# Kernel optimization log

Measured on AMD Instinct MI355X. Metric: run time of the kernel, lower is better.

Reference implementation:

```python
import jax, jax.numpy as jnp
import numpy as np

N_ENT = 50000
N_REL = 500
N_DIM = 256
K = 4            # num_blocks; n_arity = 3 -> arch has K**3 = 64 entries
B = 1024


def setup_inputs() -> dict:
    key = jax.random.key(0)
    k0, k1, k2, k3 = jax.random.split(key, 4)
    facts = jax.random.randint(k0, (B, 3), 0, N_REL)          # head, tail, rela (all < n_rel <= n_ent)
    arch = jax.random.randint(k1, (K ** 3,), 0, 3)            # selects op in {0, 1, -1}
    ent_w = jax.random.normal(k2, (N_ENT, N_DIM), dtype=jnp.float32) * 0.05  # xavier-ish scale
    rel_w = jax.random.normal(k3, (N_REL, N_DIM), dtype=jnp.float32) * 0.05
    return {
        "facts": facts,
        "arch": arch,
        "ent_w": ent_w,
        "rel_w": rel_w,
        "bne_gamma": jnp.ones((N_DIM,), jnp.float32),
        "bne_beta": jnp.zeros((N_DIM,), jnp.float32),
        "bnr_gamma": jnp.ones((N_DIM,), jnp.float32),
        "bnr_beta": jnp.zeros((N_DIM,), jnp.float32),
    }


def _bn(x, gamma, beta, eps=1e-5):
    # BatchNorm1d in training mode: biased batch statistics over the batch dim.
    m = jnp.mean(x, axis=0)
    v = jnp.var(x, axis=0)
    return (x - m) * jax.lax.rsqrt(v + eps) * gamma + beta


def _bce(p, y):
    # torch F.binary_cross_entropy clamps log terms at -100
    logp = jnp.maximum(jnp.log(p), -100.0)
    log1mp = jnp.maximum(jnp.log1p(-p), -100.0)
    return -jnp.mean(y * logp + (1.0 - y) * log1mp)


def reference(facts, arch, ent_w, rel_w, bne_gamma, bne_beta, bnr_gamma, bnr_beta):
    L = N_DIM // K
    h, t, r = facts[:, 0], facts[:, 1], facts[:, 2]
    # separate BN calls for head / tail batches, as in the torch code (dropout is eval-mode identity)
    he = _bn(ent_w[h], bne_gamma, bne_beta).reshape(-1, K, L)   # [B, K, L]
    te = _bn(ent_w[t], bne_gamma, bne_beta).reshape(-1, K, L)
    re = _bn(rel_w[r], bnr_gamma, bnr_beta).reshape(-1, K, L)
    # alpha[i,j,k] = ops[op_idx[i*K*K + j*K + k]] in {0, 1, -1}
    alpha = jnp.asarray([0.0, 1.0, -1.0], dtype=ent_w.dtype)[arch].reshape(K, K, K)
    # fused extend + inner_vec + inner_alpha_bi + sum-over-blocks:
    # last_idx=2 (head side, rela x tail): vec[b,k,l] = sum_{i,j} alpha[i,j,k] r[b,i,l] t[b,j,l]
    head_vec = jnp.einsum('ijk,bil,bjl->bkl', alpha, re, te).reshape(-1, N_DIM)
    # last_idx=1 (tail side, rela x head): vec[b,k,l] = sum_{i,j} alpha[i,k,j] r[b,i,l] h[b,j,l]
    tail_vec = jnp.einsum('ikj,bil,bjl->bkl', alpha, re, he).reshape(-1, N_DIM)
    head_p = jax.nn.softmax(head_vec @ ent_w.T, axis=1)         # [B, N_ENT]
    tail_p = jax.nn.softmax(tail_vec @ ent_w.T, axis=1)
    head_label = jax.nn.one_hot(h, N_ENT, dtype=head_p.dtype)
    tail_label = jax.nn.one_hot(t, N_ENT, dtype=tail_p.dtype)
    return _bce(head_p, head_label) + _bce(tail_p, tail_label)
```

## Files before the change

### kernel.cpp

```cpp
#include <hip/hip_runtime.h>

#define N_ENT   50000
#define N_ENT_P 50048
#define NDIM    256
#define BATCH   1024
#define MROWS   2048
#define BM      128
#define BN      128
#define BK      64
#define NTILES  391
#define NSTRIP  32
#define SHIFT   30.0f

typedef __attribute__((ext_vector_type(8))) short short8;
typedef __attribute__((ext_vector_type(4))) float f32x4;

__device__ __forceinline__ unsigned short f2bf(float f) {
  unsigned int u = __float_as_uint(f);
  u += 0x7fffu + ((u >> 16) & 1u);
  return (unsigned short)(u >> 16);
}

__device__ __forceinline__ void async16(const void* g, void* lds) {
  __builtin_amdgcn_global_load_lds(
      (const __attribute__((address_space(1))) unsigned int*)g,
      (__attribute__((address_space(3))) unsigned int*)lds,
      16, 0, 0);
}

__global__ void k_convert(const float* __restrict__ ent_w,
                          unsigned short* __restrict__ Wb) {
  int t = blockIdx.x * 256 + threadIdx.x;
  int row = t >> 6, c4 = (t & 63) << 2;
  ushort4 v;
  if (row < N_ENT) {
    float4 f = *(const float4*)(ent_w + row * NDIM + c4);
    v.x = f2bf(f.x); v.y = f2bf(f.y); v.z = f2bf(f.z); v.w = f2bf(f.w);
  } else {
    v.x = v.y = v.z = v.w = 0;
  }
  *(ushort4*)(Wb + row * NDIM + c4) = v;
}

__global__ void k_stats(const int* __restrict__ facts,
                        const float* __restrict__ ent_w,
                        const float* __restrict__ rel_w,
                        float* __restrict__ stats) {
  int seg = blockIdx.y;
  int d = threadIdx.x;
  const float* tab = (seg == 2) ? rel_w : ent_w;
  int r0 = blockIdx.x * 16;
  int idxs[16];
#pragma unroll
  for (int i = 0; i < 16; ++i) idxs[i] = facts[(r0 + i) * 3 + seg];
  float s = 0.f, s2 = 0.f;
#pragma unroll
  for (int i = 0; i < 16; ++i) {
    float v = tab[idxs[i] * NDIM + d];
    s += v; s2 += v * v;
  }
  atomicAdd(&stats[(seg * 2 + 0) * NDIM + d], s);
  atomicAdd(&stats[(seg * 2 + 1) * NDIM + d], s2);
}

__global__ void k_vectors(const int* __restrict__ facts, const int* __restrict__ arch,
                          const float* __restrict__ ent_w, const float* __restrict__ rel_w,
                          const float* __restrict__ bne_g, const float* __restrict__ bne_b,
                          const float* __restrict__ bnr_g, const float* __restrict__ bnr_b,
                          const float* __restrict__ stats,
                          unsigned short* __restrict__ HVb, float* __restrict__ zlab) {
  __shared__ float sh_he[256], sh_te[256], sh_re[256], sh_alpha[64], sh_red[16];
  int b = blockIdx.x, d = threadIdx.x;
  int h = facts[b * 3 + 0], t = facts[b * 3 + 1], r = facts[b * 3 + 2];
  const float inv = 1.0f / (float)BATCH;
  float mh = stats[0 * 256 + d] * inv, vh = stats[1 * 256 + d] * inv - mh * mh;
  float mt = stats[2 * 256 + d] * inv, vt = stats[3 * 256 + d] * inv - mt * mt;
  float mr = stats[4 * 256 + d] * inv, vr = stats[5 * 256 + d] * inv - mr * mr;
  float sch = rsqrtf(vh + 1e-5f) * bne_g[d], shh = bne_b[d] - mh * sch;
  float sct = rsqrtf(vt + 1e-5f) * bne_g[d], sht = bne_b[d] - mt * sct;
  float scr = rsqrtf(vr + 1e-5f) * bnr_g[d], shr = bnr_b[d] - mr * scr;
  sh_he[d] = ent_w[h * NDIM + d] * sch + shh;
  sh_te[d] = ent_w[t * NDIM + d] * sct + sht;
  sh_re[d] = rel_w[r * NDIM + d] * scr + shr;
  if (d < 64) {
    int a = arch[d];
    sh_alpha[d] = (a == 0) ? 0.f : ((a == 1) ? 1.f : -1.f);
  }
  __syncthreads();
  int k = d >> 6, l = d & 63;
  float hv = 0.f, tv = 0.f;
#pragma unroll
  for (int i = 0; i < 4; ++i) {
    float re_i = sh_re[i * 64 + l];
#pragma unroll
    for (int j = 0; j < 4; ++j) {
      hv += sh_alpha[i * 16 + j * 4 + k] * re_i * sh_te[j * 64 + l];
      tv += sh_alpha[i * 16 + k * 4 + j] * re_i * sh_he[j * 64 + l];
    }
  }
  HVb[b * NDIM + d] = f2bf(hv);
  HVb[(BATCH + b) * NDIM + d] = f2bf(tv);
  float ph = hv * ent_w[h * NDIM + d];
  float pt = tv * ent_w[t * NDIM + d];
  for (int m = 1; m < 64; m <<= 1) { ph += __shfl_xor(ph, m); pt += __shfl_xor(pt, m); }
  int wid = d >> 6;
  if ((d & 63) == 0) { sh_red[wid] = ph; sh_red[8 + wid] = pt; }
  __syncthreads();
  if (d == 0) {
    zlab[b] = sh_red[0] + sh_red[1] + sh_red[2] + sh_red[3];
    zlab[BATCH + b] = sh_red[8] + sh_red[9] + sh_red[10] + sh_red[11];
  }
}

__global__ void __launch_bounds__(256, 2)
k_gemm(const unsigned short* __restrict__ HVb, const unsigned short* __restrict__ Wb,
       float* __restrict__ m1, float* __restrict__ m2) {
  __shared__ __align__(16) unsigned short As[BM * BK];
  __shared__ __align__(16) unsigned short Bs[BN * BK];
  const int tid = threadIdx.x;
  const int lane = tid & 63, wid = tid >> 6;
  const int L = blockIdx.x;
  const int xcd = L & 7, r = L >> 3;
  const int strip = xcd * 4 + (r >> 4);
  const int bm = (r & 15) * BM;
  const int wm = (wid & 1) * 64, wn = (wid >> 1) * 64;
  const int q = lane >> 4, ln = lane & 15;

  float ps1[4][4] = {}, ps2[4][4] = {};

  for (int nt = strip; nt < NTILES; nt += NSTRIP) {
    const int bn = nt * BN;
    f32x4 acc[4][4] = {};
    for (int kc = 0; kc < NDIM; kc += BK) {
      __syncthreads();
#pragma unroll
      for (int c = 0; c < 4; ++c) {
        int G = (wid * 4 + c) * 64 + lane;
        int row = G >> 3, slot = G & 7;
        int kg = slot ^ (row & 7);
        async16(HVb + (bm + row) * NDIM + kc + kg * 8,
                (char*)As + (wid * 4 + c) * 1024);
        async16(Wb + (bn + row) * NDIM + kc + kg * 8,
                (char*)Bs + (wid * 4 + c) * 1024);
      }
      __syncthreads();
#pragma unroll
      for (int kk = 0; kk < BK; kk += 32) {
        short8 a[4], bb[4];
        int kg = (kk >> 3) + q;
#pragma unroll
        for (int mi = 0; mi < 4; ++mi) {
          int row = wm + mi * 16 + ln;
          a[mi] = *(const short8*)((const char*)As + row * 128 + ((kg ^ (row & 7)) << 4));
        }
#pragma unroll
        for (int ni = 0; ni < 4; ++ni) {
          int row = wn + ni * 16 + ln;
          bb[ni] = *(const short8*)((const char*)Bs + row * 128 + ((kg ^ (row & 7)) << 4));
        }
#pragma unroll
        for (int mi = 0; mi < 4; ++mi)
#pragma unroll
          for (int ni = 0; ni < 4; ++ni)
            acc[mi][ni] = __builtin_amdgcn_mfma_f32_16x16x32_bf16(a[mi], bb[ni], acc[mi][ni], 0, 0, 0);
      }
    }
#pragma unroll
    for (int mi = 0; mi < 4; ++mi)
#pragma unroll
      for (int reg = 0; reg < 4; ++reg) {
        float s1 = 0.f, s2 = 0.f;
#pragma unroll
        for (int ni = 0; ni < 4; ++ni) {
          float e1 = __expf(acc[mi][ni][reg] - SHIFT);
          s1 += e1; s2 += e1 * e1;
        }
        ps1[mi][reg] += s1;
        ps2[mi][reg] += s2;
      }
  }

#pragma unroll
  for (int mi = 0; mi < 4; ++mi)
#pragma unroll
    for (int reg = 0; reg < 4; ++reg) {
      float s1 = ps1[mi][reg], s2 = ps2[mi][reg];
      for (int m = 1; m < 16; m <<= 1) { s1 += __shfl_xor(s1, m); s2 += __shfl_xor(s2, m); }
      if (ln == 0) {
        int grow = bm + wm + mi * 16 + q * 4 + reg;
        atomicAdd(&m1[grow], s1);
        atomicAdd(&m2[grow], s2);
      }
    }
}

__global__ void k_finalize(const float* __restrict__ m1, const float* __restrict__ m2,
                           const float* __restrict__ zlab, float* __restrict__ out) {
  __shared__ float red[16];
  int tid = threadIdx.x;
  float local = 0.f;
  for (int r = tid; r < MROWS; r += 1024) {
    float M1 = m1[r];
    float lse = SHIFT + logf(M1);
    float zl = zlab[r];
    float lp = fmaxf(zl - lse, -100.f);
    float pl = __expf(zl - lse);
    float l1m = fmaxf(log1pf(-pl), -100.f);
    float iM1 = 1.f / M1;
    float r2 = m2[r] * iM1 * iM1;
    float series = -(1.f + 0.5f * r2);
    local += lp - l1m + series;
  }
  for (int m = 1; m < 64; m <<= 1) local += __shfl_xor(local, m);
  if ((tid & 63) == 0) red[tid >> 6] = local;
  __syncthreads();
  if (tid == 0) {
    float s = 0.f;
    for (int i = 0; i < 16; ++i) s += red[i];
    out[0] = -s / ((float)BATCH * (float)N_ENT);
  }
}

extern "C" void kernel_launch(void* const* d_in, const int* in_sizes, int n_in,
                              void* d_out, int out_size, void* d_ws, size_t ws_size,
                              hipStream_t stream) {
  const int* facts = (const int*)d_in[0];
  const int* arch = (const int*)d_in[1];
  const float* ent_w = (const float*)d_in[2];
  const float* rel_w = (const float*)d_in[3];
  const float* bne_g = (const float*)d_in[4];
  const float* bne_b = (const float*)d_in[5];
  const float* bnr_g = (const float*)d_in[6];
  const float* bnr_b = (const float*)d_in[7];
  char* ws = (char*)d_ws;
  float* stats = (float*)ws;
  float* m1 = (float*)(ws + 6144);
  float* m2 = (float*)(ws + 14336);
  float* zlab = (float*)(ws + 22528);
  unsigned short* HVb = (unsigned short*)(ws + 30720);
  unsigned short* Wb = (unsigned short*)(ws + 30720 + 1048576);

  hipMemsetAsync(ws, 0, 22528, stream);
  k_convert<<<dim3((N_ENT_P * 64) / 256), dim3(256), 0, stream>>>(ent_w, Wb);
  k_stats<<<dim3(64, 3), dim3(256), 0, stream>>>(facts, ent_w, rel_w, stats);
  k_vectors<<<dim3(BATCH), dim3(256), 0, stream>>>(facts, arch, ent_w, rel_w,
                                                   bne_g, bne_b, bnr_g, bnr_b,
                                                   stats, HVb, zlab);
  k_gemm<<<dim3(512), dim3(256), 0, stream>>>(HVb, Wb, m1, m2);
  k_finalize<<<dim3(1), dim3(1024), 0, stream>>>(m1, m2, zlab, (float*)d_out);
}
```

Baseline: 174.9 us.

## Switch GEMM to FP8 MFMA with register-resident A and fused prep kernel

```diff
diff --git a/kernel.cpp b/kernel.cpp
--- a/kernel.cpp
+++ b/kernel.cpp
@@ -7,19 +7,14 @@
 #define MROWS   2048
 #define BM      128
 #define BN      128
-#define BK      64
 #define NTILES  391
-#define NSTRIP  32
+#define NSTRIP  64
+#define NCONV   6256
 #define SHIFT   30.0f
-
-typedef __attribute__((ext_vector_type(8))) short short8;
+#define BSCALE  16.0f
+#define INVBSC  0.0625f
+
 typedef __attribute__((ext_vector_type(4))) float f32x4;
-
-__device__ __forceinline__ unsigned short f2bf(float f) {
-  unsigned int u = __float_as_uint(f);
-  u += 0x7fffu + ((u >> 16) & 1u);
-  return (unsigned short)(u >> 16);
-}
 
 __device__ __forceinline__ void async16(const void* g, void* lds) {
   __builtin_amdgcn_global_load_lds(
@@ -28,39 +23,47 @@
       16, 0, 0);
 }
 
-__global__ void k_convert(const float* __restrict__ ent_w,
-                          unsigned short* __restrict__ Wb) {
-  int t = blockIdx.x * 256 + threadIdx.x;
-  int row = t >> 6, c4 = (t & 63) << 2;
-  ushort4 v;
-  if (row < N_ENT) {
-    float4 f = *(const float4*)(ent_w + row * NDIM + c4);
-    v.x = f2bf(f.x); v.y = f2bf(f.y); v.z = f2bf(f.z); v.w = f2bf(f.w);
+__global__ void k_prep(const float* __restrict__ ent_w,
+                       const int* __restrict__ facts,
+                       const float* __restrict__ rel_w,
+                       unsigned char* __restrict__ Wf8,
+                       float* __restrict__ stats) {
+  int bid = blockIdx.x;
+  if (bid < NCONV) {
+    int t = bid * 256 + threadIdx.x;
+    int row = t >> 5, c8 = (t & 31) << 3;
+    int2 out;
+    if (row < N_ENT) {
+      const float4* p = (const float4*)(ent_w + row * NDIM + c8);
+      float4 f0 = p[0], f1 = p[1];
+      int lo = 0, hi = 0;
+      lo = __builtin_amdgcn_cvt_pk_fp8_f32(f0.x * BSCALE, f0.y * BSCALE, lo, false);
+      lo = __builtin_amdgcn_cvt_pk_fp8_f32(f0.z * BSCALE, f0.w * BSCALE, lo, true);
+      hi = __builtin_amdgcn_cvt_pk_fp8_f32(f1.x * BSCALE, f1.y * BSCALE, hi, false);
+      hi = __builtin_amdgcn_cvt_pk_fp8_f32(f1.z * BSCALE, f1.w * BSCALE, hi, true);
+      out.x = lo; out.y = hi;
+    } else {
+      out.x = out.y = 0;
+    }
+    *(int2*)(Wf8 + row * NDIM + c8) = out;
   } else {
-    v.x = v.y = v.z = v.w = 0;
-  }
-  *(ushort4*)(Wb + row * NDIM + c4) = v;
-}
-
-__global__ void k_stats(const int* __restrict__ facts,
-                        const float* __restrict__ ent_w,
-                        const float* __restrict__ rel_w,
-                        float* __restrict__ stats) {
-  int seg = blockIdx.y;
-  int d = threadIdx.x;
-  const float* tab = (seg == 2) ? rel_w : ent_w;
-  int r0 = blockIdx.x * 16;
-  int idxs[16];
-#pragma unroll
-  for (int i = 0; i < 16; ++i) idxs[i] = facts[(r0 + i) * 3 + seg];
-  float s = 0.f, s2 = 0.f;
-#pragma unroll
-  for (int i = 0; i < 16; ++i) {
-    float v = tab[idxs[i] * NDIM + d];
-    s += v; s2 += v * v;
-  }
-  atomicAdd(&stats[(seg * 2 + 0) * NDIM + d], s);
-  atomicAdd(&stats[(seg * 2 + 1) * NDIM + d], s2);
+    int sb = bid - NCONV;
+    int seg = sb >> 6;
+    int d = threadIdx.x;
+    const float* tab = (seg == 2) ? rel_w : ent_w;
+    int r0 = (sb & 63) * 16;
+    int idxs[16];
+#pragma unroll
+    for (int i = 0; i < 16; ++i) idxs[i] = facts[(r0 + i) * 3 + seg];
+    float s = 0.f, s2 = 0.f;
+#pragma unroll
+    for (int i = 0; i < 16; ++i) {
+      float v = tab[idxs[i] * NDIM + d];
+      s += v; s2 += v * v;
+    }
+    atomicAdd(&stats[(seg * 2 + 0) * NDIM + d], s);
+    atomicAdd(&stats[(seg * 2 + 1) * NDIM + d], s2);
+  }
 }
 
 __global__ void k_vectors(const int* __restrict__ facts, const int* __restrict__ arch,
@@ -68,7 +71,7 @@
                           const float* __restrict__ bne_g, const float* __restrict__ bne_b,
                           const float* __restrict__ bnr_g, const float* __restrict__ bnr_b,
                           const float* __restrict__ stats,
-                          unsigned short* __restrict__ HVb, float* __restrict__ zlab) {
+                          unsigned char* __restrict__ HVf8, float* __restrict__ zlab) {
   __shared__ float sh_he[256], sh_te[256], sh_re[256], sh_alpha[64], sh_red[16];
   int b = blockIdx.x, d = threadIdx.x;
   int h = facts[b * 3 + 0], t = facts[b * 3 + 1], r = facts[b * 3 + 2];
@@ -98,8 +101,10 @@
       tv += sh_alpha[i * 16 + k * 4 + j] * re_i * sh_he[j * 64 + l];
     }
   }
-  HVb[b * NDIM + d] = f2bf(hv);
-  HVb[(BATCH + b) * NDIM + d] = f2bf(tv);
+  HVf8[b * NDIM + d] =
+      (unsigned char)(__builtin_amdgcn_cvt_pk_fp8_f32(hv, hv, 0, false) & 0xff);
+  HVf8[(BATCH + b) * NDIM + d] =
+      (unsigned char)(__builtin_amdgcn_cvt_pk_fp8_f32(tv, tv, 0, false) & 0xff);
   float ph = hv * ent_w[h * NDIM + d];
   float pt = tv * ent_w[t * NDIM + d];
   for (int m = 1; m < 64; m <<= 1) { ph += __shfl_xor(ph, m); pt += __shfl_xor(pt, m); }
@@ -112,58 +117,58 @@
   }
 }
 
-__global__ void __launch_bounds__(256, 2)
-k_gemm(const unsigned short* __restrict__ HVb, const unsigned short* __restrict__ Wb,
+__global__ void __launch_bounds__(256, 3)
+k_gemm(const unsigned char* __restrict__ HVf8, const unsigned char* __restrict__ Wf8,
        float* __restrict__ m1, float* __restrict__ m2) {
-  __shared__ __align__(16) unsigned short As[BM * BK];
-  __shared__ __align__(16) unsigned short Bs[BN * BK];
+  __shared__ __align__(16) unsigned char Bs[BN * NDIM];
+  __shared__ float psm[2][128][17];
   const int tid = threadIdx.x;
   const int lane = tid & 63, wid = tid >> 6;
   const int L = blockIdx.x;
-  const int xcd = L & 7, r = L >> 3;
-  const int strip = xcd * 4 + (r >> 4);
-  const int bm = (r & 15) * BM;
+  const int xcd = L & 7, rr = L >> 3;
+  const int strip = xcd * 8 + (rr >> 4);
+  const int bm = (rr & 15) * BM;
   const int wm = (wid & 1) * 64, wn = (wid >> 1) * 64;
   const int q = lane >> 4, ln = lane & 15;
 
-  float ps1[4][4] = {}, ps2[4][4] = {};
+  for (int i = tid; i < 2 * 128 * 17; i += 256) ((float*)psm)[i] = 0.f;
+
+  long a[4][8];
+#pragma unroll
+  for (int mi = 0; mi < 4; ++mi) {
+    const unsigned char* ap = HVf8 + (bm + wm + mi * 16 + ln) * NDIM + q * 8;
+#pragma unroll
+    for (int s = 0; s < 8; ++s) a[mi][s] = *(const long*)(ap + s * 32);
+  }
 
   for (int nt = strip; nt < NTILES; nt += NSTRIP) {
     const int bn = nt * BN;
     f32x4 acc[4][4] = {};
-    for (int kc = 0; kc < NDIM; kc += BK) {
-      __syncthreads();
-#pragma unroll
-      for (int c = 0; c < 4; ++c) {
-        int G = (wid * 4 + c) * 64 + lane;
-        int row = G >> 3, slot = G & 7;
-        int kg = slot ^ (row & 7);
-        async16(HVb + (bm + row) * NDIM + kc + kg * 8,
-                (char*)As + (wid * 4 + c) * 1024);
-        async16(Wb + (bn + row) * NDIM + kc + kg * 8,
-                (char*)Bs + (wid * 4 + c) * 1024);
+    __syncthreads();
+#pragma unroll
+    for (int c = 0; c < 8; ++c) {
+      int G = (wid * 8 + c) * 64 + lane;
+      int row = G >> 4, sr = G & 15;
+      int g = (sr & 8) | ((sr & 7) ^ (row & 7));
+      async16(Wf8 + (bn + row) * NDIM + g * 16, (char*)Bs + G * 16);
+    }
+    __syncthreads();
+#pragma unroll
+    for (int st = 0; st < 8; ++st) {
+      long bb[4];
+      int g = st * 2 + (q >> 1), sub = (q & 1) * 8;
+#pragma unroll
+      for (int ni = 0; ni < 4; ++ni) {
+        int row = wn + ni * 16 + ln;
+        int slot = (g & 8) | ((g & 7) ^ (row & 7));
+        bb[ni] = *(const long*)(Bs + row * 256 + slot * 16 + sub);
       }
-      __syncthreads();
-#pragma unroll
-      for (int kk = 0; kk < BK; kk += 32) {
-        short8 a[4], bb[4];
-        int kg = (kk >> 3) + q;
-#pragma unroll
-        for (int mi = 0; mi < 4; ++mi) {
-          int row = wm + mi * 16 + ln;
-          a[mi] = *(const short8*)((const char*)As + row * 128 + ((kg ^ (row & 7)) << 4));
-        }
-#pragma unroll
-        for (int ni = 0; ni < 4; ++ni) {
-          int row = wn + ni * 16 + ln;
-          bb[ni] = *(const short8*)((const char*)Bs + row * 128 + ((kg ^ (row & 7)) << 4));
-        }
-#pragma unroll
-        for (int mi = 0; mi < 4; ++mi)
-#pragma unroll
-          for (int ni = 0; ni < 4; ++ni)
-            acc[mi][ni] = __builtin_amdgcn_mfma_f32_16x16x32_bf16(a[mi], bb[ni], acc[mi][ni], 0, 0, 0);
-      }
+#pragma unroll
+      for (int mi = 0; mi < 4; ++mi)
+#pragma unroll
+        for (int ni = 0; ni < 4; ++ni)
+          acc[mi][ni] = __builtin_amdgcn_mfma_f32_16x16x32_fp8_fp8(
+              a[mi][st], bb[ni], acc[mi][ni], 0, 0, 0);
     }
 #pragma unroll
     for (int mi = 0; mi < 4; ++mi)
@@ -172,26 +177,22 @@
         float s1 = 0.f, s2 = 0.f;
 #pragma unroll
         for (int ni = 0; ni < 4; ++ni) {
-          float e1 = __expf(acc[mi][ni][reg] - SHIFT);
+          float e1 = __expf(acc[mi][ni][reg] * INVBSC - SHIFT);
           s1 += e1; s2 += e1 * e1;
         }
-        ps1[mi][reg] += s1;
-        ps2[mi][reg] += s2;
+        int row = wm + mi * 16 + q * 4 + reg;
+        atomicAdd(&psm[0][row][ln], s1);
+        atomicAdd(&psm[1][row][ln], s2);
       }
   }
 
-#pragma unroll
-  for (int mi = 0; mi < 4; ++mi)
-#pragma unroll
-    for (int reg = 0; reg < 4; ++reg) {
-      float s1 = ps1[mi][reg], s2 = ps2[mi][reg];
-      for (int m = 1; m < 16; m <<= 1) { s1 += __shfl_xor(s1, m); s2 += __shfl_xor(s2, m); }
-      if (ln == 0) {
-        int grow = bm + wm + mi * 16 + q * 4 + reg;
-        atomicAdd(&m1[grow], s1);
-        atomicAdd(&m2[grow], s2);
-      }
-    }
+  __syncthreads();
+  int row = tid & 127;
+  int arr = tid >> 7;
+  float s = 0.f;
+#pragma unroll
+  for (int c = 0; c < 16; ++c) s += psm[arr][row][c];
+  atomicAdd(arr ? &m2[bm + row] : &m1[bm + row], s);
 }
 
 __global__ void k_finalize(const float* __restrict__ m1, const float* __restrict__ m2,
@@ -237,15 +238,14 @@
   float* m1 = (float*)(ws + 6144);
   float* m2 = (float*)(ws + 14336);
   float* zlab = (float*)(ws + 22528);
-  unsigned short* HVb = (unsigned short*)(ws + 30720);
-  unsigned short* Wb = (unsigned short*)(ws + 30720 + 1048576);
+  unsigned char* HVf8 = (unsigned char*)(ws + 30720);
+  unsigned char* Wf8 = (unsigned char*)(ws + 30720 + 524288);
 
   hipMemsetAsync(ws, 0, 22528, stream);
-  k_convert<<<dim3((N_ENT_P * 64) / 256), dim3(256), 0, stream>>>(ent_w, Wb);
-  k_stats<<<dim3(64, 3), dim3(256), 0, stream>>>(facts, ent_w, rel_w, stats);
+  k_prep<<<dim3(NCONV + 192), dim3(256), 0, stream>>>(ent_w, facts, rel_w, Wf8, stats);
   k_vectors<<<dim3(BATCH), dim3(256), 0, stream>>>(facts, arch, ent_w, rel_w,
                                                    bne_g, bne_b, bnr_g, bnr_b,
-                                                   stats, HVb, zlab);
-  k_gemm<<<dim3(512), dim3(256), 0, stream>>>(HVb, Wb, m1, m2);
+                                                   stats, HVf8, zlab);
+  k_gemm<<<dim3(1024), dim3(256), 0, stream>>>(HVf8, Wf8, m1, m2);
   k_finalize<<<dim3(1), dim3(1024), 0, stream>>>(m1, m2, zlab, (float*)d_out);
 }
```

Result: slower. 455.5 us (+160.5%).
